# Optimization experiments

Hardware: AMD Instinct MI355X
Metric: run time of the kernel (lower is better)

## Reference

```python
import jax, jax.numpy as jnp
import numpy as np

_B, _Q, _D, _H, _L, _F, _C, _HM = 8, 100, 256, 8, 9, 2048, 151, 112


def setup_inputs():
    key = jax.random.key(0)
    ks = list(jax.random.split(key, 40)); ki = [0]
    def nk():
        k = ks[ki[0]]; ki[0] += 1; return k
    def r(shape, s=1.0):
        return jax.random.normal(nk(), shape, jnp.float32) * s
    z, o = jnp.zeros, jnp.ones
    return {
        'mask_features': r((_B, _D, _HM, _HM)),
        'mem0': r((_B, _D, 14, 14)), 'mem1': r((_B, _D, 28, 28)), 'mem2': r((_B, _D, 56, 56)),
        'query_feat': r((_Q, _D), 0.02), 'query_embed': r((_Q, _D), 0.02),
        'ca_wqkv': r((_L, 3, _D, _D), 0.02), 'ca_bqkv': z((_L, 3, _D)),
        'ca_wo': r((_L, _D, _D), 0.02), 'ca_bo': z((_L, _D)),
        'ca_ln_s': o((_L, _D)), 'ca_ln_b': z((_L, _D)),
        'sa_wqkv': r((_L, 3, _D, _D), 0.02), 'sa_bqkv': z((_L, 3, _D)),
        'sa_wo': r((_L, _D, _D), 0.02), 'sa_bo': z((_L, _D)),
        'sa_ln_s': o((_L, _D)), 'sa_ln_b': z((_L, _D)),
        'ffn_w1': r((_L, _D, _F), 0.02), 'ffn_b1': z((_L, _F)),
        'ffn_w2': r((_L, _F, _D), 0.02), 'ffn_b2': z((_L, _D)),
        'ffn_ln_s': o((_L, _D)), 'ffn_ln_b': z((_L, _D)),
        'dec_ln_s': o((_D,)), 'dec_ln_b': z((_D,)),
        'me_w1': r((_D, _D), 0.02), 'me_b1': z((_D,)),
        'me_w2': r((_D, _D), 0.02), 'me_b2': z((_D,)),
        'me_w3': r((_D, _D), 0.02), 'me_b3': z((_D,)),
        'cls_w': r((_D, _C), 0.02), 'cls_b': z((_C,)),
    }


def _ln(x, s, b, eps=1e-5):
    m = x.mean(-1, keepdims=True)
    v = ((x - m) ** 2).mean(-1, keepdims=True)
    return (x - m) * jax.lax.rsqrt(v + eps) * s + b


def _mha(q, k, v, wqkv, bqkv, wo, bo, bias):
    # q: [B,Nq,D]; k,v: [B,Nk,D]; bias: [B,1,Nq,Nk] additive (-1e9 = masked) or None
    B, Nq, D = q.shape
    hd = D // _H
    qh = (q @ wqkv[0] + bqkv[0]).reshape(B, Nq, _H, hd)
    kh = (k @ wqkv[1] + bqkv[1]).reshape(B, -1, _H, hd)
    vh = (v @ wqkv[2] + bqkv[2]).reshape(B, -1, _H, hd)
    scores = jnp.einsum('bqhd,bkhd->bhqk', qh, kh) / np.sqrt(hd).astype(np.float32)
    if bias is not None:
        scores = scores + bias
    attn = jax.nn.softmax(scores, axis=-1)
    out = jnp.einsum('bhqk,bkhd->bqhd', attn, vh).reshape(B, Nq, D)
    return out @ wo + bo


def _attn_bias(prev_mask, hw):
    # prev_mask: [B,Q,Hm,Wm] raw logits -> additive bias [B,1,Q,H*W]
    B, Q = prev_mask.shape[:2]
    r = jax.image.resize(prev_mask, (B, Q) + hw, 'bilinear')  # align_corners=False
    ignore = (jax.nn.sigmoid(r) < 0.5).reshape(B, Q, -1)      # True = masked out
    fully = jnp.all(ignore, axis=-1, keepdims=True)           # un-mask fully-masked rows
    ignore = jnp.where(fully, False, ignore)
    return jnp.where(ignore, jnp.float32(-1e9), jnp.float32(0.0))[:, None]


def _forward(mask_features, mem0, mem1, mem2, query_feat, query_embed,
             ca_wqkv, ca_bqkv, ca_wo, ca_bo, ca_ln_s, ca_ln_b,
             sa_wqkv, sa_bqkv, sa_wo, sa_bo, sa_ln_s, sa_ln_b,
             ffn_w1, ffn_b1, ffn_w2, ffn_b2, ffn_ln_s, ffn_ln_b,
             dec_ln_s, dec_ln_b, me_w1, me_b1, me_w2, me_b2, me_w3, me_b3,
             cls_w, cls_b):
    B, D, Hm, Wm = mask_features.shape
    Q = query_feat.shape[0]
    mems = [(m.reshape(B, D, -1).transpose(0, 2, 1), m.shape[2:]) for m in (mem0, mem1, mem2)]
    mask_flat = mask_features.reshape(B, D, -1).transpose(0, 2, 1)  # [B,Hm*Wm,D]
    q = jnp.broadcast_to((query_feat + query_embed)[None], (B, Q, D))
    prev = None
    for i in range(_L):
        mem, hw = mems[i % 3]
        bias = _attn_bias(prev, hw) if prev is not None else None
        q = _ln(q + _mha(q, mem, mem, ca_wqkv[i], ca_bqkv[i], ca_wo[i], ca_bo[i], bias), ca_ln_s[i], ca_ln_b[i])
        q = _ln(q + _mha(q, q, q, sa_wqkv[i], sa_bqkv[i], sa_wo[i], sa_bo[i], None), sa_ln_s[i], sa_ln_b[i])
        h = jax.nn.relu(q @ ffn_w1[i] + ffn_b1[i]) @ ffn_w2[i] + ffn_b2[i]
        q = _ln(q + h, ffn_ln_s[i], ffn_ln_b[i])
        nq = _ln(q, dec_ln_s, dec_ln_b)
        me = jax.nn.relu(jax.nn.relu(nq @ me_w1 + me_b1) @ me_w2 + me_b2) @ me_w3 + me_b3
        pred_mask = jnp.einsum('bqd,bpd->bqp', me, mask_flat).reshape(B, Q, Hm, Wm)
        prev = jax.lax.stop_gradient(pred_mask)
    pred_logits = nq @ cls_w + cls_b
    return pred_logits, pred_mask


def reference(mask_features, mem0, mem1, mem2, query_feat, query_embed,
              ca_wqkv, ca_bqkv, ca_wo, ca_bo, ca_ln_s, ca_ln_b,
              sa_wqkv, sa_bqkv, sa_wo, sa_bo, sa_ln_s, sa_ln_b,
              ffn_w1, ffn_b1, ffn_w2, ffn_b2, ffn_ln_s, ffn_ln_b,
              dec_ln_s, dec_ln_b, me_w1, me_b1, me_w2, me_b2, me_w3, me_b3,
              cls_w, cls_b):
    return _forward(mask_features, mem0, mem1, mem2, query_feat, query_embed,
                    ca_wqkv, ca_bqkv, ca_wo, ca_bo, ca_ln_s, ca_ln_b,
                    sa_wqkv, sa_bqkv, sa_wo, sa_bo, sa_ln_s, sa_ln_b,
                    ffn_w1, ffn_b1, ffn_w2, ffn_b2, ffn_ln_s, ffn_ln_b,
                    dec_ln_s, dec_ln_b, me_w1, me_b1, me_w2, me_b2, me_w3, me_b3,
                    cls_w, cls_b)
```

## Files before the change

kernel.cpp:

```cpp
#include <hip/hip_runtime.h>
#include <cmath>

#define B_ 8
#define Q_ 100
#define D_ 256
#define H_ 8
#define HD_ 32
#define L_ 9
#define F_ 2048
#define C_ 151
#define HM_ 112
#define PMAX_ 3136
#define KT_ 128
#define RECSZ 544

typedef __attribute__((ext_vector_type(4))) short s4v;
typedef __attribute__((ext_vector_type(8))) short s8v;
typedef __attribute__((ext_vector_type(4))) float f4v;

__device__ __forceinline__ unsigned short f2bf(float x) {
  unsigned int u = __float_as_uint(x);
  return (unsigned short)((u + 0x7fffu + ((u >> 16) & 1u)) >> 16);
}
__device__ __forceinline__ float bf2f(unsigned short h) {
  return __uint_as_float(((unsigned int)h) << 16);
}
__device__ __forceinline__ void split2(float x, short& h, short& l) {
  unsigned short hb = f2bf(x);
  float r = x - bf2f(hb);
  h = (short)hb;
  l = (short)f2bf(r);
}

__device__ __forceinline__ float block_sum(float v, float* red) {
  int t = threadIdx.x;
  red[t] = v; __syncthreads();
  for (int s = 128; s > 0; s >>= 1) {
    if (t < s) red[t] += red[t + s];
    __syncthreads();
  }
  float r = red[0]; __syncthreads();
  return r;
}

__global__ __launch_bounds__(256) void initq_kernel(const float* __restrict__ qf,
                                                    const float* __restrict__ qe,
                                                    float* __restrict__ q) {
  int idx = blockIdx.x * 256 + threadIdx.x;
  int qd = idx % (Q_ * D_);
  q[idx] = qf[qd] + qe[qd];
}

template <int OH>
__device__ __forceinline__ void resize_one(const float* __restrict__ pl,
                                           float* __restrict__ out,
                                           float* htmp, float* wbuf, int* sbuf, int t) {
  constexpr int RATIO = HM_ / OH;
  constexpr int TAPS = 2 * RATIO;
  constexpr float INVR = 1.f / (float)RATIO;
  if (t < OH) {
    float s = ((float)t + 0.5f) * RATIO - 0.5f;
    int x0 = (int)floorf(s - RATIO) + 1;
    sbuf[t] = x0;
    float ws = 0.f;
#pragma unroll
    for (int si = 0; si < TAPS; ++si) {
      int x = x0 + si;
      float w = (x >= 0 && x < HM_) ? 1.f - fabsf(s - (float)x) * INVR : 0.f;
      wbuf[t * TAPS + si] = w;
      ws += w;
    }
    float inv = 1.f / ws;
#pragma unroll
    for (int si = 0; si < TAPS; ++si) wbuf[t * TAPS + si] *= inv;
  }
  __syncthreads();
  for (int idx = t; idx < OH * HM_; idx += 256) {
    int oc = idx / HM_, row = idx - oc * HM_;
    int x0 = sbuf[oc];
    const float* wr = &wbuf[oc * TAPS];
    const float* pr = pl + row * HM_;
    float acc0 = 0.f, acc1 = 0.f;
#pragma unroll
    for (int si = 0; si < TAPS; si += 2) {
      int xa = min(max(x0 + si, 0), HM_ - 1);
      int xb = min(max(x0 + si + 1, 0), HM_ - 1);
      acc0 += wr[si] * pr[xa];
      acc1 += wr[si + 1] * pr[xb];
    }
    htmp[oc * 114 + row] = acc0 + acc1;
  }
  __syncthreads();
  for (int idx = t; idx < OH * OH; idx += 256) {
    int oy = idx / OH, ox = idx - oy * OH;
    int y0 = sbuf[oy];
    const float* wr = &wbuf[oy * TAPS];
    const float* hp = &htmp[ox * 114];
    float acc0 = 0.f, acc1 = 0.f;
#pragma unroll
    for (int si = 0; si < TAPS; si += 2) {
      int ya = min(max(y0 + si, 0), HM_ - 1);
      int yb = min(max(y0 + si + 1, 0), HM_ - 1);
      acc0 += wr[si] * hp[ya];
      acc1 += wr[si + 1] * hp[yb];
    }
    out[idx] = acc0 + acc1;
  }
  __syncthreads();
}

__global__ __launch_bounds__(256) void resize3_kernel(
    const float* __restrict__ mf, float* __restrict__ r0,
    float* __restrict__ r1, float* __restrict__ r2) {
  __shared__ float htmp[56 * 114];
  __shared__ float wbuf[224];
  __shared__ int sbuf[56];
  const int bd = blockIdx.x;
  const float* pl = mf + (size_t)bd * (HM_ * HM_);
  const int t = threadIdx.x;
  resize_one<14>(pl, r0 + (size_t)bd * 196, htmp, wbuf, sbuf, t);
  resize_one<28>(pl, r1 + (size_t)bd * 784, htmp, wbuf, sbuf, t);
  resize_one<56>(pl, r2 + (size_t)bd * 3136, htmp, wbuf, sbuf, t);
}

__global__ __launch_bounds__(256) void tsplit_kernel(
    const float* __restrict__ in, short* __restrict__ out,
    int K, int N, long long ibs, long long obs) {
  __shared__ float tile[32][33];
  const int z = blockIdx.z;
  const int nb = blockIdx.x * 32, kb = blockIdx.y * 32;
  const float* I = in + (size_t)z * ibs;
  short* O = out + (size_t)z * obs;
  const int t = threadIdx.x;
  {
    const int r = t >> 3, c = (t & 7) * 4;
    const int gk = kb + r;
#pragma unroll
    for (int j = 0; j < 4; ++j) {
      int gn = nb + c + j;
      tile[r][c + j] = (gk < K && gn < N) ? I[(size_t)gk * N + gn] : 0.f;
    }
  }
  __syncthreads();
  {
    const int nr = t >> 3, kc = (t & 7) * 4;
    const int gn = nb + nr;
    if (gn < N) {
#pragma unroll
      for (int j = 0; j < 4; ++j) {
        int gk = kb + kc + j;
        if (gk < K) {
          short h, l; split2(tile[kc + j][nr], h, l);
          O[(size_t)gn * 2 * K + gk] = h;
          O[(size_t)gn * 2 * K + K + gk] = l;
        }
      }
    }
  }
}

__global__ __launch_bounds__(256) void tsplitp_kernel(
    const float* __restrict__ in, short* __restrict__ out,
    int K, int N, int Na, long long ibs, long long obs) {
  __shared__ float tile[32][33];
  const int z = blockIdx.z;
  const int nb = blockIdx.x * 32, kb = blockIdx.y * 32;
  const float* I = in + (size_t)z * ibs;
  short* O = out + (size_t)z * obs;
  const int t = threadIdx.x;
  {
    const int r = t >> 3, c = (t & 7) * 4;
    const int gk = kb + r;
#pragma unroll
    for (int j = 0; j < 4; ++j) {
      int gn = nb + c + j;
      tile[r][c + j] = (gk < K && gn < N) ? I[(size_t)gk * N + gn] : 0.f;
    }
  }
  __syncthreads();
  {
    const int nr = t >> 3, kc = (t & 7) * 4;
    const int gn = nb + nr;
    if (gn < Na) {
#pragma unroll
      for (int j = 0; j < 4; ++j) {
        int gk = kb + kc + j;
        if (gk < K) {
          short h, l; split2(tile[kc + j][nr], h, l);
          O[(size_t)gn * 2 * K + gk] = h;
          O[(size_t)gn * 2 * K + K + gk] = l;
        }
      }
    }
  }
}

__device__ __forceinline__ s8v ldfrag(const short* p) {
  s4v lo = *(const s4v*)p;
  s4v hi = *(const s4v*)(p + 16);
  return __builtin_shufflevector(lo, hi, 0, 1, 2, 3, 4, 5, 6, 7);
}

template <int BM, int AMODE, int WMODE, bool RELU, int OUT>
__global__ __launch_bounds__(256) void mgemm_kernel(
    const void* __restrict__ Ap, const void* __restrict__ Wp,
    const float* __restrict__ bias, void* __restrict__ Cv,
    int M, int N, int K,
    long long Abs, long long Wbs, long long Cbs, int ldc, int swap) {
  constexpr int MI = BM / 32;
  __shared__ short Ah[BM * 36], Al[BM * 36], Wh[128 * 36], Wl[128 * 36];
  const int z = blockIdx.z;
  const int bx = swap ? blockIdx.y : blockIdx.x;
  const int by = swap ? blockIdx.x : blockIdx.y;
  const int n0 = bx * 128, m0 = by * BM;
  const int t = threadIdx.x;
  const int lane = t & 63;
  const int wave = t >> 6;
  const int wm = wave >> 1, wn = wave & 1;
  const int lr = lane & 15, lg = lane >> 4;
  f4v acc[MI][4];
#pragma unroll
  for (int i = 0; i < MI; ++i)
#pragma unroll
    for (int j = 0; j < 4; ++j) acc[i][j] = (f4v){0.f, 0.f, 0.f, 0.f};

  for (int k0 = 0; k0 < K; k0 += 32) {
    if (AMODE == 0) {
      const float* A = (const float*)Ap + (size_t)z * Abs;
      if (BM == 64) {
        const int arow = t >> 2;
        const int kc = (t & 3) * 8;
        float x[8];
        if (m0 + arow < M) {
          const float* ap = A + (size_t)(m0 + arow) * K + k0 + kc;
          *(f4v*)&x[0] = *(const f4v*)ap;
          *(f4v*)&x[4] = *(const f4v*)(ap + 4);
        } else {
#pragma unroll
          for (int e = 0; e < 8; ++e) x[e] = 0.f;
        }
        s4v h0, h1, l0, l1;
#pragma unroll
        for (int e = 0; e < 4; ++e) { short hh, ll; split2(x[e], hh, ll); h0[e] = hh; l0[e] = ll; }
#pragma unroll
        for (int e = 0; e < 4; ++e) { short hh, ll; split2(x[4 + e], hh, ll); h1[e] = hh; l1[e] = ll; }
        *(s4v*)&Ah[arow * 36 + kc] = h0; *(s4v*)&Ah[arow * 36 + kc + 4] = h1;
        *(s4v*)&Al[arow * 36 + kc] = l0; *(s4v*)&Al[arow * 36 + kc + 4] = l1;
      } else {
        const int arow = t >> 3;
        const int kc = (t & 7) * 4;
        float x[4];
        if (m0 + arow < M) {
          *(f4v*)&x[0] = *(const f4v*)(A + (size_t)(m0 + arow) * K + k0 + kc);
        } else {
#pragma unroll
          for (int e = 0; e < 4; ++e) x[e] = 0.f;
        }
        s4v h0, l0;
#pragma unroll
        for (int e = 0; e < 4; ++e) { short hh, ll; split2(x[e], hh, ll); h0[e] = hh; l0[e] = ll; }
        *(s4v*)&Ah[arow * 36 + kc] = h0;
        *(s4v*)&Al[arow * 36 + kc] = l0;
      }
    } else {
      const short* A2 = (const short*)Ap + (size_t)z * Abs;
      const int arow = t >> 2;
      const int c = t & 3, sel = c >> 1, ko = (c & 1) * 16;
      s8v v0 = {0, 0, 0, 0, 0, 0, 0, 0}, v1 = {0, 0, 0, 0, 0, 0, 0, 0};
      if (m0 + arow < M) {
        const short* ap = A2 + (size_t)(m0 + arow) * (2 * K) + sel * K + k0 + ko;
        v0 = *(const s8v*)ap;
        v1 = *(const s8v*)(ap + 8);
      }
      short* dst = sel ? Al : Ah;
      *(s4v*)&dst[arow * 36 + ko] = __builtin_shufflevector(v0, v0, 0, 1, 2, 3);
      *(s4v*)&dst[arow * 36 + ko + 4] = __builtin_shufflevector(v0, v0, 4, 5, 6, 7);
      *(s4v*)&dst[arow * 36 + ko + 8] = __builtin_shufflevector(v1, v1, 0, 1, 2, 3);
      *(s4v*)&dst[arow * 36 + ko + 12] = __builtin_shufflevector(v1, v1, 4, 5, 6, 7);
    }
    if (WMODE == 0) {
      const short* W2 = (const short*)Wp + (size_t)z * Wbs;
      const int n = t >> 1, sel = t & 1;
      const short* wp = W2 + (size_t)(n0 + n) * (2 * K) + sel * K + k0;
      short* dst = sel ? Wl : Wh;
#pragma unroll
      for (int j = 0; j < 4; ++j) {
        s8v v = *(const s8v*)(wp + j * 8);
        *(s4v*)&dst[n * 36 + j * 8] = __builtin_shufflevector(v, v, 0, 1, 2, 3);
        *(s4v*)&dst[n * 36 + j * 8 + 4] = __builtin_shufflevector(v, v, 4, 5, 6, 7);
      }
    } else {
      const float* W = (const float*)Wp + (size_t)z * Wbs;
      const int kr = t >> 3, c0 = (t & 7) * 16;
      const float* wp = W + (size_t)(k0 + kr) * N + n0 + c0;
      float x[16];
#pragma unroll
      for (int j = 0; j < 4; ++j) *(f4v*)&x[j * 4] = *(const f4v*)(wp + j * 4);
#pragma unroll
      for (int j = 0; j < 16; ++j) {
        short hh, ll; split2(x[j], hh, ll);
        Wh[(c0 + j) * 36 + kr] = hh;
        Wl[(c0 + j) * 36 + kr] = ll;
      }
    }
    __syncthreads();
    s8v whf[4], wlf[4];
#pragma unroll
    for (int ni = 0; ni < 4; ++ni) {
      whf[ni] = ldfrag(&Wh[(wn * 64 + ni * 16 + lr) * 36 + 4 * lg]);
      wlf[ni] = ldfrag(&Wl[(wn * 64 + ni * 16 + lr) * 36 + 4 * lg]);
    }
#pragma unroll
    for (int mi = 0; mi < MI; ++mi) {
      s8v ah = ldfrag(&Ah[(wm * (BM / 2) + mi * 16 + lr) * 36 + 4 * lg]);
      s8v al = ldfrag(&Al[(wm * (BM / 2) + mi * 16 + lr) * 36 + 4 * lg]);
#pragma unroll
      for (int ni = 0; ni < 4; ++ni) {
        acc[mi][ni] = __builtin_amdgcn_mfma_f32_16x16x32_bf16(ah, whf[ni], acc[mi][ni], 0, 0, 0);
        acc[mi][ni] = __builtin_amdgcn_mfma_f32_16x16x32_bf16(al, whf[ni], acc[mi][ni], 0, 0, 0);
        acc[mi][ni] = __builtin_amdgcn_mfma_f32_16x16x32_bf16(ah, wlf[ni], acc[mi][ni], 0, 0, 0);
      }
    }
    __syncthreads();
  }
  float* Cf = (float*)Cv + (size_t)z * Cbs;
  unsigned short* Ch = (unsigned short*)Cv + (size_t)z * Cbs;
#pragma unroll
  for (int mi = 0; mi < MI; ++mi) {
#pragma unroll
    for (int i = 0; i < 4; ++i) {
      int row = m0 + wm * (BM / 2) + mi * 16 + 4 * lg + i;
      if (row >= M) continue;
#pragma unroll
      for (int ni = 0; ni < 4; ++ni) {
        int col = n0 + wn * 64 + ni * 16 + lr;
        float v = acc[mi][ni][i] + (bias ? bias[col] : 0.f);
        if (RELU) v = fmaxf(v, 0.f);
        if (OUT == 0) Cf[(size_t)row * ldc + col] = v;
        else Ch[(size_t)row * ldc + col] = f2bf(v);
      }
    }
  }
}

__global__ __launch_bounds__(256) void maskhead_kernel(
    const float* __restrict__ q, const float* __restrict__ lns,
    const float* __restrict__ lnb, const short* __restrict__ W123,
    const float* __restrict__ b1, const float* __restrict__ b2,
    const float* __restrict__ b3,
    float* __restrict__ nqout, float* __restrict__ me3out) {
  __shared__ float Xb[16 * 264], Yb[16 * 264];
  __shared__ short Ah[16 * 36], Al[16 * 36], Wh[256 * 36], Wl[256 * 36];
  const int r0 = blockIdx.x * 16;
  const int t = threadIdx.x;
  const int lane = t & 63, w = t >> 6;
  const int lr = lane & 15, lg = lane >> 4;
#pragma unroll
  for (int rr = 0; rr < 4; ++rr) {
    int row = w * 4 + rr;
    int grow = r0 + row;
    f4v v = *((const f4v*)(q + (size_t)grow * D_) + lane);
    float sum = v[0] + v[1] + v[2] + v[3];
#pragma unroll
    for (int off = 32; off > 0; off >>= 1) sum += __shfl_xor(sum, off, 64);
    float mean = sum * (1.f / D_);
    float c0 = v[0] - mean, c1 = v[1] - mean, c2 = v[2] - mean, c3 = v[3] - mean;
    float vs = c0 * c0 + c1 * c1 + c2 * c2 + c3 * c3;
#pragma unroll
    for (int off = 32; off > 0; off >>= 1) vs += __shfl_xor(vs, off, 64);
    float inv = rsqrtf(vs * (1.f / D_) + 1e-5f);
    f4v sv = *((const f4v*)lns + lane);
    f4v bv = *((const f4v*)lnb + lane);
    f4v o;
    o[0] = c0 * inv * sv[0] + bv[0];
    o[1] = c1 * inv * sv[1] + bv[1];
    o[2] = c2 * inv * sv[2] + bv[2];
    o[3] = c3 * inv * sv[3] + bv[3];
    *(f4v*)&Xb[row * 264 + lane * 4] = o;
    *((f4v*)(nqout + (size_t)grow * D_) + lane) = o;
  }
  __syncthreads();
  float* src = Xb;
  float* dst = Yb;
  for (int s = 0; s < 3; ++s) {
    const short* Ws = W123 + (size_t)s * 131072;
    const float* bs = (s == 0) ? b1 : ((s == 1) ? b2 : b3);
    f4v acc[4];
#pragma unroll
    for (int j = 0; j < 4; ++j) acc[j] = (f4v){0.f, 0.f, 0.f, 0.f};
    for (int k0 = 0; k0 < 256; k0 += 32) {
      {
        int idx = t * 2;
        int row = idx >> 5, kc = idx & 31;
        short h0, l0, h1, l1;
        split2(src[row * 264 + k0 + kc], h0, l0);
        split2(src[row * 264 + k0 + kc + 1], h1, l1);
        Ah[row * 36 + kc] = h0; Ah[row * 36 + kc + 1] = h1;
        Al[row * 36 + kc] = l0; Al[row * 36 + kc + 1] = l1;
      }
      {
        const short* wp = Ws + (size_t)t * 512 + k0;
#pragma unroll
        for (int j = 0; j < 8; ++j)
          *(s4v*)&Wh[t * 36 + j * 4] = *(const s4v*)(wp + j * 4);
        const short* wpl = wp + 256;
#pragma unroll
        for (int j = 0; j < 8; ++j)
          *(s4v*)&Wl[t * 36 + j * 4] = *(const s4v*)(wpl + j * 4);
      }
      __syncthreads();
      s8v ah = ldfrag(&Ah[lr * 36 + 4 * lg]);
      s8v al = ldfrag(&Al[lr * 36 + 4 * lg]);
#pragma unroll
      for (int ni = 0; ni < 4; ++ni) {
        s8v wh = ldfrag(&Wh[(w * 64 + ni * 16 + lr) * 36 + 4 * lg]);
        s8v wl = ldfrag(&Wl[(w * 64 + ni * 16 + lr) * 36 + 4 * lg]);
        acc[ni] = __builtin_amdgcn_mfma_f32_16x16x32_bf16(ah, wh, acc[ni], 0, 0, 0);
        acc[ni] = __builtin_amdgcn_mfma_f32_16x16x32_bf16(al, wh, acc[ni], 0, 0, 0);
        acc[ni] = __builtin_amdgcn_mfma_f32_16x16x32_bf16(ah, wl, acc[ni], 0, 0, 0);
      }
      __syncthreads();
    }
#pragma unroll
    for (int ni = 0; ni < 4; ++ni) {
#pragma unroll
      for (int i = 0; i < 4; ++i) {
        int row = 4 * lg + i;
        int col = w * 64 + ni * 16 + lr;
        float v = acc[ni][i] + bs[col];
        if (s < 2) v = fmaxf(v, 0.f);
        dst[row * 264 + col] = v;
      }
    }
    __syncthreads();
    float* tmpp = src; src = dst; dst = tmpp;
  }
  for (int o = t; o < 16 * 256; o += 256) {
    int row = o >> 8, col = o & 255;
    me3out[(size_t)(r0 + row) * D_ + col] = src[row * 264 + col];
  }
}

__global__ __launch_bounds__(256) void gemm32_kernel(
    const float* __restrict__ A, const float* __restrict__ W,
    const float* __restrict__ bias, float* __restrict__ C,
    int M, int N, int K) {
  __shared__ float As[16][65];
  __shared__ float Ws[16][65];
  const int n0 = blockIdx.x * 64, m0 = blockIdx.y * 64;
  const int t = threadIdx.x;
  const int tm = t >> 4, tn = t & 15;
  float acc[4][4] = {};
  for (int k0 = 0; k0 < K; k0 += 16) {
#pragma unroll
    for (int l = 0; l < 4; ++l) {
      int idx = t + l * 256;
      int am = idx >> 4, ak = idx & 15;
      int gm = m0 + am, gk = k0 + ak;
      As[ak][am] = (gm < M) ? A[(size_t)gm * K + gk] : 0.f;
      int wk = idx >> 6, wn = idx & 63;
      int gn = n0 + wn, gk2 = k0 + wk;
      Ws[wk][wn] = (gn < N) ? W[(size_t)gk2 * N + gn] : 0.f;
    }
    __syncthreads();
#pragma unroll
    for (int kk = 0; kk < 16; ++kk) {
      float a[4], b[4];
#pragma unroll
      for (int i = 0; i < 4; ++i) a[i] = As[kk][tm * 4 + i];
#pragma unroll
      for (int j = 0; j < 4; ++j) b[j] = Ws[kk][tn * 4 + j];
#pragma unroll
      for (int i = 0; i < 4; ++i)
#pragma unroll
        for (int j = 0; j < 4; ++j) acc[i][j] += a[i] * b[j];
    }
    __syncthreads();
  }
#pragma unroll
  for (int i = 0; i < 4; ++i) {
    int gm = m0 + tm * 4 + i;
    if (gm >= M) continue;
#pragma unroll
    for (int j = 0; j < 4; ++j) {
      int gn = n0 + tn * 4 + j;
      if (gn >= N) continue;
      C[(size_t)gm * N + gn] = acc[i][j] + bias[gn];
    }
  }
}

template <bool RES>
__global__ __launch_bounds__(256) void ln_kernel(const float* __restrict__ x,
                                                 const float* __restrict__ r,
                                                 const float* __restrict__ s,
                                                 const float* __restrict__ b,
                                                 float* __restrict__ out, int nrows) {
  const int wave = threadIdx.x >> 6, lane = threadIdx.x & 63;
  const int row = blockIdx.x * 4 + wave;
  if (row >= nrows) return;
  f4v v = *((const f4v*)(x + (size_t)row * D_) + lane);
  if (RES) {
    f4v rv = *((const f4v*)(r + (size_t)row * D_) + lane);
    v[0] += rv[0]; v[1] += rv[1]; v[2] += rv[2]; v[3] += rv[3];
  }
  float sum = v[0] + v[1] + v[2] + v[3];
#pragma unroll
  for (int off = 32; off > 0; off >>= 1) sum += __shfl_xor(sum, off, 64);
  float mean = sum * (1.f / D_);
  float c0 = v[0] - mean, c1 = v[1] - mean, c2 = v[2] - mean, c3 = v[3] - mean;
  float vs = c0 * c0 + c1 * c1 + c2 * c2 + c3 * c3;
#pragma unroll
  for (int off = 32; off > 0; off >>= 1) vs += __shfl_xor(vs, off, 64);
  float inv = rsqrtf(vs * (1.f / D_) + 1e-5f);
  f4v sv = *((const f4v*)s + lane);
  f4v bv = *((const f4v*)b + lane);
  f4v o;
  o[0] = c0 * inv * sv[0] + bv[0];
  o[1] = c1 * inv * sv[1] + bv[1];
  o[2] = c2 * inv * sv[2] + bv[2];
  o[3] = c3 * inv * sv[3] + bv[3];
  *((f4v*)(out + (size_t)row * D_) + lane) = o;
}

template <bool BIAS, bool KVBF16, bool SPLIT>
__global__ __launch_bounds__(256) void mattn_kernel(
    const float* __restrict__ qb, int ldq,
    const void* __restrict__ kbv, int ldk,
    const void* __restrict__ vbv, int ldv,
    const unsigned int* __restrict__ bits,
    float* __restrict__ outp, int P, int Pw, int tps, int S) {
  __shared__ __align__(16) short Kt[128 * 40];
  __shared__ __align__(16) short Vt[32 * 132];
  __shared__ __align__(16) short Pt[4 * 16 * 36];
  __shared__ unsigned int bb[64];
  __shared__ float Msh[4][16], Lsh[4][16];
  float* Osh = (float*)Kt;
  const int b = blockIdx.x >> 3, h = blockIdx.x & 7;
  const int q0 = blockIdx.y * 16;
  const int seg = blockIdx.z;
  const int kbeg = seg * tps * KT_;
  const int kend = min(P, kbeg + tps * KT_);
  const int t = threadIdx.x;
  const int lane = t & 63, w = t >> 6;
  const int lr = lane & 15, lg = lane >> 4;
  const float scale = 0.17677669529663687f;

  s8v qhf, qlf;
  {
    int qrow = q0 + lr; if (qrow >= Q_) qrow = Q_ - 1;
    const float* qp = qb + (size_t)(b * Q_ + qrow) * ldq + h * HD_;
#pragma unroll
    for (int e = 0; e < 8; ++e) {
      int d = 4 * lg + (e & 3) + 16 * (e >> 2);
      short hh, ll; split2(qp[d], hh, ll);
      qhf[e] = hh; qlf[e] = ll;
    }
  }
  float mreg[4], lreg[4];
  f4v accO0 = (f4v){0.f, 0.f, 0.f, 0.f}, accO1 = (f4v){0.f, 0.f, 0.f, 0.f};
#pragma unroll
  for (int i = 0; i < 4; ++i) { mreg[i] = -3.0e38f; lreg[i] = 0.f; }

  for (int k0 = kbeg; k0 < kend; k0 += KT_) {
    {
      const int key = t >> 1, dh = (t & 1) * 16;
      const int gk = k0 + key;
      s8v ka = {0,0,0,0,0,0,0,0}, kb2 = {0,0,0,0,0,0,0,0};
      s8v va = {0,0,0,0,0,0,0,0}, vb2 = {0,0,0,0,0,0,0,0};
      if (gk < kend) {
        if (KVBF16) {
          const unsigned short* kp = (const unsigned short*)kbv + (size_t)(b * P + gk) * ldk + h * HD_ + dh;
          const unsigned short* vp = (const unsigned short*)vbv + (size_t)(b * P + gk) * ldv + h * HD_ + dh;
          ka = *(const s8v*)kp; kb2 = *(const s8v*)(kp + 8);
          va = *(const s8v*)vp; vb2 = *(const s8v*)(vp + 8);
        } else {
          const float* kp = (const float*)kbv + (size_t)(b * P + gk) * ldk + h * HD_ + dh;
          const float* vp = (const float*)vbv + (size_t)(b * P + gk) * ldv + h * HD_ + dh;
#pragma unroll
          for (int j = 0; j < 8; ++j) {
            ka[j] = (short)f2bf(kp[j]); kb2[j] = (short)f2bf(kp[8 + j]);
            va[j] = (short)f2bf(vp[j]); vb2[j] = (short)f2bf(vp[8 + j]);
          }
        }
      }
      *(s8v*)&Kt[key * 40 + dh] = ka;
      *(s8v*)&Kt[key * 40 + dh + 8] = kb2;
#pragma unroll
      for (int j = 0; j < 8; ++j) {
        Vt[(dh + j) * 132 + key] = va[j];
        Vt[(dh + 8 + j) * 132 + key] = vb2[j];
      }
    }
    if (BIAS && t < 64) {
      int qq = t >> 2, wi = t & 3;
      int gr = q0 + qq, gw = (k0 >> 5) + wi;
      bb[t] = (gr < Q_ && gw < Pw) ? bits[(size_t)(b * Q_ + gr) * Pw + gw] : 0u;
    }
    __syncthreads();
    s8v kf0 = ldfrag(&Kt[(w * 32 + lr) * 40 + 4 * lg]);
    s8v kf1 = ldfrag(&Kt[(w * 32 + 16 + lr) * 40 + 4 * lg]);
    f4v accS0 = (f4v){0.f, 0.f, 0.f, 0.f}, accS1 = (f4v){0.f, 0.f, 0.f, 0.f};
    accS0 = __builtin_amdgcn_mfma_f32_16x16x32_bf16(qhf, kf0, accS0, 0, 0, 0);
    accS0 = __builtin_amdgcn_mfma_f32_16x16x32_bf16(qlf, kf0, accS0, 0, 0, 0);
    accS1 = __builtin_amdgcn_mfma_f32_16x16x32_bf16(qhf, kf1, accS1, 0, 0, 0);
    accS1 = __builtin_amdgcn_mfma_f32_16x16x32_bf16(qlf, kf1, accS1, 0, 0, 0);
    const int gk0 = k0 + w * 32 + lr;
#pragma unroll
    for (int i = 0; i < 4; ++i) {
      float s0 = accS0[i] * scale, s1 = accS1[i] * scale;
      if (BIAS) {
        unsigned int word = bb[(4 * lg + i) * 4 + w];
        if ((word >> lr) & 1u) s0 += -1e9f;
        if ((word >> (16 + lr)) & 1u) s1 += -1e9f;
      }
      if (gk0 >= kend) s0 = -3.0e38f;
      if (gk0 + 16 >= kend) s1 = -3.0e38f;
      float rm = fmaxf(s0, s1);
#pragma unroll
      for (int off = 1; off < 16; off <<= 1) rm = fmaxf(rm, __shfl_xor(rm, off, 64));
      float mn = fmaxf(mreg[i], rm);
      float corr = __expf(mreg[i] - mn);
      mreg[i] = mn;
      float p0 = __expf(s0 - mn), p1 = __expf(s1 - mn);
      lreg[i] = lreg[i] * corr + p0 + p1;
      accO0[i] *= corr;
      accO1[i] *= corr;
      Pt[w * 576 + (4 * lg + i) * 36 + lr] = (short)f2bf(p0);
      Pt[w * 576 + (4 * lg + i) * 36 + 16 + lr] = (short)f2bf(p1);
    }
    s8v pf = ldfrag(&Pt[w * 576 + lr * 36 + 4 * lg]);
    s8v vf0 = ldfrag(&Vt[lr * 132 + w * 32 + 4 * lg]);
    s8v vf1 = ldfrag(&Vt[(16 + lr) * 132 + w * 32 + 4 * lg]);
    accO0 = __builtin_amdgcn_mfma_f32_16x16x32_bf16(pf, vf0, accO0, 0, 0, 0);
    accO1 = __builtin_amdgcn_mfma_f32_16x16x32_bf16(pf, vf1, accO1, 0, 0, 0);
    __syncthreads();
  }
#pragma unroll
  for (int i = 0; i < 4; ++i) {
    float lv = lreg[i];
#pragma unroll
    for (int off = 1; off < 16; off <<= 1) lv += __shfl_xor(lv, off, 64);
    if (lr == 0) { Msh[w][4 * lg + i] = mreg[i]; Lsh[w][4 * lg + i] = lv; }
  }
#pragma unroll
  for (int i = 0; i < 4; ++i) {
    Osh[w * 528 + (4 * lg + i) * 33 + lr] = accO0[i];
    Osh[w * 528 + (4 * lg + i) * 33 + 16 + lr] = accO1[i];
  }
  __syncthreads();
  float* part = SPLIT
      ? outp + ((size_t)((blockIdx.x * gridDim.y + blockIdx.y) * S + seg)) * RECSZ
      : nullptr;
  for (int o = t; o < 512; o += 256) {
    int qq = o >> 5, d = o & 31;
    float M = fmaxf(fmaxf(Msh[0][qq], Msh[1][qq]), fmaxf(Msh[2][qq], Msh[3][qq]));
    float lt = 0.f, Ov = 0.f;
#pragma unroll
    for (int w4 = 0; w4 < 4; ++w4) {
      float wt = __expf(Msh[w4][qq] - M);
      lt += wt * Lsh[w4][qq];
      Ov += wt * Osh[w4 * 528 + qq * 33 + d];
    }
    if (SPLIT) {
      if (d == 0) { part[qq] = M; part[16 + qq] = lt; }
      part[32 + qq * 32 + d] = Ov;
    } else if (q0 + qq < Q_) {
      outp[(size_t)(b * Q_ + q0 + qq) * D_ + h * HD_ + d] = Ov / lt;
    }
  }
}

__global__ __launch_bounds__(256) void attncomb_kernel(
    const float* __restrict__ part, float* __restrict__ out, int S, int nqt) {
  const int row = blockIdx.x;
  const int b = row / Q_, qq = row % Q_;
  const int t = threadIdx.x;
  const int h = t >> 5, d = t & 31;
  const int qt = qq >> 4, r = qq & 15;
  const float* base = part + ((size_t)((b * 8 + h) * nqt + qt) * S) * RECSZ;
  float M = -3.0e38f;
  for (int s = 0; s < S; ++s) M = fmaxf(M, base[(size_t)s * RECSZ + r]);
  float lt = 0.f, Ov = 0.f;
  for (int s = 0; s < S; ++s) {
    const float* rec = base + (size_t)s * RECSZ;
    float w = __expf(rec[r] - M);
    lt += w * rec[16 + r];
    Ov += w * rec[32 + r * 32 + d];
  }
  out[(size_t)row * D_ + h * HD_ + d] = Ov / lt;
}

__global__ __launch_bounds__(256) void packbits_kernel(
    const float* __restrict__ r, unsigned int* __restrict__ bias, int P, int ldr) {
  __shared__ float red[256];
  __shared__ unsigned int bw[128];
  const int row = blockIdx.x;
  const int b = row / Q_, qq = row % Q_;
  const int t = threadIdx.x;
  const float* src = r + (size_t)b * Q_ * ldr + (size_t)qq * ldr;
  const int Pw = (P + 31) >> 5;
  float nign = 0.f;
  for (int p = t; p < P; p += 256)
    if (!(src[p] < 0.f)) nign += 1.f;
  float tot = block_sum(nign, red);
  bool fully = (tot == 0.f);
  for (int w = t; w < Pw; w += 256) bw[w] = 0u;
  __syncthreads();
  if (!fully) {
    for (int p = t; p < P; p += 256) {
      if (src[p] < 0.f) atomicOr(&bw[p >> 5], 1u << (p & 31));
    }
  }
  __syncthreads();
  unsigned int* dst = bias + (size_t)row * Pw;
  for (int w = t; w < Pw; w += 256) dst[w] = bw[w];
}

static inline void mg(hipStream_t st, int bm, int amode, int wmode, bool relu,
                      const void* A, const void* W, const float* bias, void* C,
                      int M, int N, int K, int Z,
                      long long Abs, long long Wbs, long long Cbs, int ldc) {
  dim3 g(N / 128, (M + bm - 1) / bm, Z);
  if (bm == 32) {
    if (relu)
      mgemm_kernel<32, 0, 0, true, 0><<<g, 256, 0, st>>>(A, W, bias, C, M, N, K, Abs, Wbs, Cbs, ldc, 0);
    else
      mgemm_kernel<32, 0, 0, false, 0><<<g, 256, 0, st>>>(A, W, bias, C, M, N, K, Abs, Wbs, Cbs, ldc, 0);
  } else {
    if (amode == 1)
      mgemm_kernel<64, 1, 0, false, 1><<<g, 256, 0, st>>>(A, W, bias, C, M, N, K, Abs, Wbs, Cbs, ldc, 0);
    else
      mgemm_kernel<64, 0, 0, false, 0><<<g, 256, 0, st>>>(A, W, bias, C, M, N, K, Abs, Wbs, Cbs, ldc, 0);
  }
}

extern "C" void kernel_launch(void* const* d_in, const int* in_sizes, int n_in,
                              void* d_out, int out_size, void* d_ws, size_t ws_size,
                              hipStream_t stream) {
  const float* mask_features = (const float*)d_in[0];
  const float* mem[3] = {(const float*)d_in[1], (const float*)d_in[2], (const float*)d_in[3]};
  const float* qf = (const float*)d_in[4];
  const float* qe = (const float*)d_in[5];
  const float* ca_wqkv = (const float*)d_in[6];
  const float* ca_bqkv = (const float*)d_in[7];
  const float* ca_wo = (const float*)d_in[8];
  const float* ca_bo = (const float*)d_in[9];
  const float* ca_ln_s = (const float*)d_in[10];
  const float* ca_ln_b = (const float*)d_in[11];
  const float* sa_wqkv = (const float*)d_in[12];
  const float* sa_bqkv = (const float*)d_in[13];
  const float* sa_wo = (const float*)d_in[14];
  const float* sa_bo = (const float*)d_in[15];
  const float* sa_ln_s = (const float*)d_in[16];
  const float* sa_ln_b = (const float*)d_in[17];
  const float* ffn_w1 = (const float*)d_in[18];
  const float* ffn_b1 = (const float*)d_in[19];
  const float* ffn_w2 = (const float*)d_in[20];
  const float* ffn_b2 = (const float*)d_in[21];
  const float* ffn_ln_s = (const float*)d_in[22];
  const float* ffn_ln_b = (const float*)d_in[23];
  const float* dec_ln_s = (const float*)d_in[24];
  const float* dec_ln_b = (const float*)d_in[25];
  const float* me_w1 = (const float*)d_in[26];
  const float* me_b1 = (const float*)d_in[27];
  const float* me_w2 = (const float*)d_in[28];
  const float* me_b2 = (const float*)d_in[29];
  const float* me_w3 = (const float*)d_in[30];
  const float* me_b3 = (const float*)d_in[31];
  const float* cls_w = (const float*)d_in[32];
  const float* cls_b = (const float*)d_in[33];

  float* out_logits = (float*)d_out;
  float* out_mask = (float*)d_out + (size_t)800 * C_;

  float* fws = (float*)d_ws;
  float* q      = fws; fws += (size_t)800 * D_;
  float* qh     = fws; fws += (size_t)800 * D_;
  float* attn_o = fws; fws += (size_t)800 * D_;
  float* tmp    = fws; fws += (size_t)800 * D_;
  float* nq     = fws; fws += (size_t)800 * D_;
  float* me3    = fws; fws += (size_t)800 * D_;
  float* kvbuf  = fws; fws += (size_t)B_ * PMAX_ * 256;
  float* qkvbuf = fws; fws += (size_t)800 * 768;
  float* biasb  = fws; fws += (size_t)800 * 128;
  float* ffnh   = fws; fws += (size_t)B_ * Q_ * F_;
  float* part   = fws; fws += (size_t)64 * 7 * 3 * RECSZ;
  float* rmf0   = fws; fws += (size_t)B_ * 256 * 196;
  float* rmf1   = fws; fws += (size_t)B_ * 256 * 784;
  float* rmf2   = fws; fws += (size_t)B_ * 256 * 3136;
  float* rbias  = fws; fws += (size_t)B_ * Q_ * 3200;

  unsigned short* kvb = (unsigned short*)kvbuf;
  unsigned int* biasbits = (unsigned int*)biasb;

  short* sws = (short*)fws;
  short* W2ca  = sws; sws += (size_t)27 * 256 * 512;
  short* W2sa  = sws; sws += (size_t)27 * 256 * 512;
  short* W2cao = sws; sws += (size_t)9 * 256 * 512;
  short* W2sao = sws; sws += (size_t)9 * 256 * 512;
  short* W2f1  = sws; sws += (size_t)9 * 2048 * 512;
  short* W2f2  = sws; sws += (size_t)9 * 256 * 4096;
  short* W2me  = sws; sws += (size_t)3 * 256 * 512;
  short* mem2s = sws; sws += (size_t)B_ * 3136 * 512;
  short* mem1s = sws; sws += (size_t)B_ * 784 * 512;
  short* mem0s = sws; sws += (size_t)B_ * 196 * 512;
  short* memsp[3] = {mem0s, mem1s, mem2s};
  short* rmfs0 = sws; sws += (size_t)B_ * 256 * 512;
  short* rmfs1 = sws; sws += (size_t)B_ * 896 * 512;
  short* rmfs2 = sws; sws += (size_t)B_ * 3200 * 512;
  short* rmfs[3] = {rmfs0, rmfs1, rmfs2};

  tsplit_kernel<<<dim3(8, 8, 27), 256, 0, stream>>>(ca_wqkv, W2ca, 256, 256, 65536, 131072);
  tsplit_kernel<<<dim3(8, 8, 27), 256, 0, stream>>>(sa_wqkv, W2sa, 256, 256, 65536, 131072);
  tsplit_kernel<<<dim3(8, 8, 9), 256, 0, stream>>>(ca_wo, W2cao, 256, 256, 65536, 131072);
  tsplit_kernel<<<dim3(8, 8, 9), 256, 0, stream>>>(sa_wo, W2sao, 256, 256, 65536, 131072);
  tsplit_kernel<<<dim3(64, 8, 9), 256, 0, stream>>>(ffn_w1, W2f1, 256, 2048, 524288, 1048576);
  tsplit_kernel<<<dim3(8, 64, 9), 256, 0, stream>>>(ffn_w2, W2f2, 2048, 256, 524288, 1048576);
  tsplit_kernel<<<dim3(8, 8, 1), 256, 0, stream>>>(me_w1, W2me, 256, 256, 0, 0);
  tsplit_kernel<<<dim3(8, 8, 1), 256, 0, stream>>>(me_w2, W2me + 131072, 256, 256, 0, 0);
  tsplit_kernel<<<dim3(8, 8, 1), 256, 0, stream>>>(me_w3, W2me + 262144, 256, 256, 0, 0);
  tsplit_kernel<<<dim3(7, 8, 8), 256, 0, stream>>>(mem[0], mem0s, 256, 196, 256 * 196, 196 * 512);
  tsplit_kernel<<<dim3(25, 8, 8), 256, 0, stream>>>(mem[1], mem1s, 256, 784, 256 * 784, 784 * 512);
  tsplit_kernel<<<dim3(98, 8, 8), 256, 0, stream>>>(mem[2], mem2s, 256, 3136, 256 * 3136, 3136 * 512);

  resize3_kernel<<<2048, 256, 0, stream>>>(mask_features, rmf0, rmf1, rmf2);
  tsplitp_kernel<<<dim3(8, 8, 8), 256, 0, stream>>>(rmf0, rmfs0, 256, 196, 256,
                                                    256 * 196, 256 * 512);
  tsplitp_kernel<<<dim3(28, 8, 8), 256, 0, stream>>>(rmf1, rmfs1, 256, 784, 896,
                                                     256 * 784, 896 * 512);
  tsplitp_kernel<<<dim3(100, 8, 8), 256, 0, stream>>>(rmf2, rmfs2, 256, 3136, 3200,
                                                      256 * 3136, 3200 * 512);

  initq_kernel<<<800, 256, 0, stream>>>(qf, qe, q);

  const int Ps[3] = {196, 784, 3136};
  const int Ppad[3] = {256, 896, 3200};
  const int Ss[3] = {1, 2, 3};
  for (int i = 0; i < L_; ++i) {
    const int mi = i % 3, P = Ps[mi];
    const int Pw = (P + 31) >> 5;
    const int S = Ss[mi];
    const int ntiles = (P + KT_ - 1) / KT_;
    const int tps = (ntiles + S - 1) / S;
    mg(stream, 32, 0, 0, false, q, W2ca + (size_t)(i * 3) * 131072, ca_bqkv + i * 768, qh,
       800, 256, 256, 1, 0, 0, 0, 256);
    mg(stream, 64, 1, 0, false, memsp[mi], W2ca + (size_t)(i * 3 + 1) * 131072,
       ca_bqkv + i * 768 + 256, kvb,
       P, 512, 256, B_, (long long)P * 512, 0, (long long)P * 512, 512);
    {
      dim3 ag(64, 7, S);
      if (S > 1) {
        if (i > 0)
          mattn_kernel<true, true, true><<<ag, 256, 0, stream>>>(
              qh, 256, kvb, 512, kvb + 256, 512, biasbits, part, P, Pw, tps, S);
        else
          mattn_kernel<false, true, true><<<ag, 256, 0, stream>>>(
              qh, 256, kvb, 512, kvb + 256, 512, nullptr, part, P, Pw, tps, S);
        attncomb_kernel<<<800, 256, 0, stream>>>(part, attn_o, S, 7);
      } else {
        if (i > 0)
          mattn_kernel<true, true, false><<<ag, 256, 0, stream>>>(
              qh, 256, kvb, 512, kvb + 256, 512, biasbits, attn_o, P, Pw, tps, S);
        else
          mattn_kernel<false, true, false><<<ag, 256, 0, stream>>>(
              qh, 256, kvb, 512, kvb + 256, 512, nullptr, attn_o, P, Pw, tps, S);
      }
    }
    mg(stream, 32, 0, 0, false, attn_o, W2cao + (size_t)i * 131072, ca_bo + i * 256, tmp,
       800, 256, 256, 1, 0, 0, 0, 256);
    ln_kernel<true><<<200, 256, 0, stream>>>(tmp, q, ca_ln_s + i * 256, ca_ln_b + i * 256, q, 800);
    mg(stream, 32, 0, 0, false, q, W2sa + (size_t)(i * 3) * 131072, sa_bqkv + i * 768, qkvbuf,
       800, 768, 256, 1, 0, 0, 0, 768);
    mattn_kernel<false, false, false><<<dim3(64, 7, 1), 256, 0, stream>>>(
        qkvbuf, 768, qkvbuf + 256, 768, qkvbuf + 512, 768, nullptr, attn_o, 100, 4, 1, 1);
    mg(stream, 32, 0, 0, false, attn_o, W2sao + (size_t)i * 131072, sa_bo + i * 256, tmp,
       800, 256, 256, 1, 0, 0, 0, 256);
    ln_kernel<true><<<200, 256, 0, stream>>>(tmp, q, sa_ln_s + i * 256, sa_ln_b + i * 256, q, 800);
    mg(stream, 32, 0, 0, true, q, W2f1 + (size_t)i * 1048576, ffn_b1 + i * 2048, ffnh,
       800, 2048, 256, 1, 0, 0, 0, 2048);
    mg(stream, 32, 0, 0, false, ffnh, W2f2 + (size_t)i * 1048576, ffn_b2 + i * 256, tmp,
       800, 256, 2048, 1, 0, 0, 0, 256);
    ln_kernel<true><<<200, 256, 0, stream>>>(tmp, q, ffn_ln_s + i * 256, ffn_ln_b + i * 256, q, 800);
    maskhead_kernel<<<50, 256, 0, stream>>>(q, dec_ln_s, dec_ln_b, W2me,
                                            me_b1, me_b2, me_b3, nq, me3);
    if (i < L_ - 1) {
      const int mn = (i + 1) % 3;
      const int Pn = Ps[mn], Pp = Ppad[mn];
      mgemm_kernel<32, 0, 0, false, 0><<<dim3(Pp / 128, 4, 8), 256, 0, stream>>>(
          me3, rmfs[mn], nullptr, rbias, 100, Pp, 256,
          (long long)100 * 256, (long long)Pp * 512, (long long)100 * Pp, Pp, 0);
      packbits_kernel<<<800, 256, 0, stream>>>(rbias, biasbits, Pn, Pp);
    } else {
      mgemm_kernel<64, 0, 1, false, 0><<<dim3(2, 98, 8), 256, 0, stream>>>(
          me3, mask_features, nullptr, out_mask, 100, 12544, 256,
          (long long)100 * 256, (long long)256 * 12544, (long long)100 * 12544, 12544, 1);
    }
  }
  gemm32_kernel<<<dim3(3, 13, 1), 256, 0, stream>>>(nq, cls_w, cls_b, out_logits, 800, C_, 256);
}
```

Measured before the change: 2.990 ms.

## Stage mask plane in shared memory and fuse separable resize passes

The resize kernel now loads each 112x112 plane into shared memory once, using vectorized float4 loads into a padded layout. All three output resolutions are then computed from that shared copy in a single 2D pass, replacing the separate horizontal and vertical passes that re-read global memory for each scale. This cuts global memory traffic and removes one barrier per scale. In exchange, each output does TAPS x TAPS multiply-adds instead of about 2 x TAPS, so arithmetic grows, notably for the 14x14 output with 16 taps. Shared memory use per block also rises to about 52 KB, which may reduce occupancy.

```diff
diff --git a/kernel.cpp b/kernel.cpp
--- a/kernel.cpp
+++ b/kernel.cpp
@@ -13,6 +13,7 @@
 #define PMAX_ 3136
 #define KT_ 128
 #define RECSZ 544
+#define PMS 116
 
 typedef __attribute__((ext_vector_type(4))) short s4v;
 typedef __attribute__((ext_vector_type(8))) short s8v;
@@ -52,9 +53,9 @@
 }
 
 template <int OH>
-__device__ __forceinline__ void resize_one(const float* __restrict__ pl,
-                                           float* __restrict__ out,
-                                           float* htmp, float* wbuf, int* sbuf, int t) {
+__device__ __forceinline__ void resize_plane(const float* __restrict__ pm,
+                                             float* __restrict__ out,
+                                             float* wbuf, int* sbuf, int t) {
   constexpr int RATIO = HM_ / OH;
   constexpr int TAPS = 2 * RATIO;
   constexpr float INVR = 1.f / (float)RATIO;
@@ -75,36 +76,27 @@
     for (int si = 0; si < TAPS; ++si) wbuf[t * TAPS + si] *= inv;
   }
   __syncthreads();
-  for (int idx = t; idx < OH * HM_; idx += 256) {
-    int oc = idx / HM_, row = idx - oc * HM_;
-    int x0 = sbuf[oc];
-    const float* wr = &wbuf[oc * TAPS];
-    const float* pr = pl + row * HM_;
-    float acc0 = 0.f, acc1 = 0.f;
-#pragma unroll
-    for (int si = 0; si < TAPS; si += 2) {
-      int xa = min(max(x0 + si, 0), HM_ - 1);
-      int xb = min(max(x0 + si + 1, 0), HM_ - 1);
-      acc0 += wr[si] * pr[xa];
-      acc1 += wr[si + 1] * pr[xb];
-    }
-    htmp[oc * 114 + row] = acc0 + acc1;
-  }
-  __syncthreads();
-  for (int idx = t; idx < OH * OH; idx += 256) {
-    int oy = idx / OH, ox = idx - oy * OH;
-    int y0 = sbuf[oy];
-    const float* wr = &wbuf[oy * TAPS];
-    const float* hp = &htmp[ox * 114];
-    float acc0 = 0.f, acc1 = 0.f;
-#pragma unroll
-    for (int si = 0; si < TAPS; si += 2) {
-      int ya = min(max(y0 + si, 0), HM_ - 1);
-      int yb = min(max(y0 + si + 1, 0), HM_ - 1);
-      acc0 += wr[si] * hp[ya];
-      acc1 += wr[si + 1] * hp[yb];
-    }
-    out[idx] = acc0 + acc1;
+  for (int p = t; p < OH * OH; p += 256) {
+    int oy = p / OH, ox = p - oy * OH;
+    int x0 = sbuf[ox], y0 = sbuf[oy];
+    const float* wx = &wbuf[ox * TAPS];
+    const float* wy = &wbuf[oy * TAPS];
+    float acc = 0.f;
+#pragma unroll
+    for (int ti = 0; ti < TAPS; ++ti) {
+      int y = min(max(y0 + ti, 0), HM_ - 1);
+      const float* pr = pm + y * PMS;
+      float ra0 = 0.f, ra1 = 0.f;
+#pragma unroll
+      for (int si = 0; si < TAPS; si += 2) {
+        int xa = min(max(x0 + si, 0), HM_ - 1);
+        int xb = min(max(x0 + si + 1, 0), HM_ - 1);
+        ra0 += wx[si] * pr[xa];
+        ra1 += wx[si + 1] * pr[xb];
+      }
+      acc += wy[ti] * (ra0 + ra1);
+    }
+    out[p] = acc;
   }
   __syncthreads();
 }
@@ -112,15 +104,20 @@
 __global__ __launch_bounds__(256) void resize3_kernel(
     const float* __restrict__ mf, float* __restrict__ r0,
     float* __restrict__ r1, float* __restrict__ r2) {
-  __shared__ float htmp[56 * 114];
+  __shared__ float pm[HM_ * PMS];
   __shared__ float wbuf[224];
   __shared__ int sbuf[56];
   const int bd = blockIdx.x;
   const float* pl = mf + (size_t)bd * (HM_ * HM_);
   const int t = threadIdx.x;
-  resize_one<14>(pl, r0 + (size_t)bd * 196, htmp, wbuf, sbuf, t);
-  resize_one<28>(pl, r1 + (size_t)bd * 784, htmp, wbuf, sbuf, t);
-  resize_one<56>(pl, r2 + (size_t)bd * 3136, htmp, wbuf, sbuf, t);
+  for (int f = t; f < (HM_ * HM_) / 4; f += 256) {
+    int row = f / 28, c = (f - row * 28) * 4;
+    *(f4v*)&pm[row * PMS + c] = ((const f4v*)pl)[f];
+  }
+  __syncthreads();
+  resize_plane<14>(pm, r0 + (size_t)bd * 196, wbuf, sbuf, t);
+  resize_plane<28>(pm, r1 + (size_t)bd * 784, wbuf, sbuf, t);
+  resize_plane<56>(pm, r2 + (size_t)bd * 3136, wbuf, sbuf, t);
 }
 
 __global__ __launch_bounds__(256) void tsplit_kernel(
```

New measurement: 2.777 ms (median of 3 runs). 7.1% less time.
